# Performance work log

Measured on AMD Instinct MI355X. Metric: run time of the kernel, lower is better.

Reference implementation:

```python
import jax, jax.numpy as jnp
import numpy as np

M = 2          # n_mix
D_K = 128      # feature dim
TEMP = float(np.sqrt(D_K))  # temperature = d_k ** 0.5


def setup_inputs() -> dict:
    key = jax.random.key(0)
    k1, k2, k3, k4 = jax.random.split(key, 4)
    BS, N, N2 = 8, 2048, 2048
    qt = jax.random.normal(k1, (BS, N, D_K), jnp.float32)
    kt = jax.random.normal(k2, (BS, N2, D_K), jnp.float32)
    vt = jax.random.normal(k3, (BS, N2, D_K), jnp.float32)
    std = M ** -0.5
    kernel = jax.random.uniform(k4, (M, D_K), jnp.float32, -std, std)
    return {"qt": qt, "kt": kt, "vt": vt, "kernel": kernel}


def reference(qt, kt, vt, kernel):
    # channels_last path of MixtureOfSoftMaxACF.call, training=False (dropout = identity)
    BS, N, dk = qt.shape
    N2 = kt.shape[1]
    d = dk // M
    # mixture prior: softmax(kernel @ mean_q^T) over axis=1 (faithful to Softmax(axis=1))
    bar_qt = jnp.mean(qt, axis=1)                       # (BS, dk)
    prior_mix = jax.nn.softmax(kernel @ bar_qt.T, axis=1)  # (m, BS)
    prior_mix = prior_mix.reshape(BS * M, 1, 1)            # row-major reshape, as in TF
    # split features into mixtures via row-major reshape (as tf.reshape does)
    q = qt.reshape(BS * M, N, d)
    k = kt.reshape(BS * M, N2, d)
    att = jnp.einsum('bnd,bmd->bnm', q, k) / TEMP        # (BS*m, N, N2)
    att = jax.nn.softmax(att, axis=2)
    att = (att * prior_mix).reshape(BS, M, N, N2).sum(axis=1)  # (BS, N, N2)
    return att @ vt                                      # (BS, N, d_v)
```

## Files before the change

kernel.cpp:

```cpp
#include <hip/hip_runtime.h>
#include <hip/hip_fp16.h>

typedef float    f32x4 __attribute__((ext_vector_type(4)));
typedef _Float16 f16x2 __attribute__((ext_vector_type(2)));
typedef _Float16 f16x4 __attribute__((ext_vector_type(4)));
typedef _Float16 f16x8 __attribute__((ext_vector_type(8)));

#define BS 8
#define NN 2048
#define DK 128
#define DM 64
#define MIXOFF (1024 * DK)
#define QSCALE 0.12751744116926208f

#define MFMA32(a, b, c) __builtin_amdgcn_mfma_f32_16x16x32_f16((a), (b), (c), 0, 0, 0)
#define EXP2(x) __builtin_amdgcn_exp2f(x)

__device__ __forceinline__ f16x2 pkrtz(float x, float y) {
  return __builtin_bit_cast(f16x2, __builtin_amdgcn_cvt_pkrtz(x, y));
}

__device__ __forceinline__ void load_lds16(const _Float16* g, _Float16* l) {
  __builtin_amdgcn_global_load_lds(
      (const __attribute__((address_space(1))) void*)(uintptr_t)g,
      (__attribute__((address_space(3))) void*)(uint32_t)(uintptr_t)l, 16, 0, 0);
}

__global__ void prep_k(const float* __restrict__ kt, _Float16* __restrict__ kh,
                       const float* __restrict__ vt, _Float16* __restrict__ vT,
                       const float* __restrict__ qt, float* __restrict__ qpart) {
  __shared__ float tile[64][65];
  __shared__ float red[256];
  int blk = blockIdx.x;
  int t = threadIdx.x;
  if (blk < 512) {
    size_t base = (size_t)blk * 4096;
#pragma unroll
    for (int j = 0; j < 4; ++j) {
      size_t i = base + j * 1024 + t * 4;
      f32x4 v = *(const f32x4*)(kt + i);
      f16x4 h;
      h[0] = (_Float16)v[0]; h[1] = (_Float16)v[1];
      h[2] = (_Float16)v[2]; h[3] = (_Float16)v[3];
      *(f16x4*)(kh + i) = h;
    }
  } else if (blk < 1024) {
    int i2 = blk - 512;
    int b = i2 >> 6;
    int rem = i2 & 63;
    int j0 = (rem & 31) * 64;
    int c0 = (rem >> 5) * 64;
    int tx = t & 63, ty = t >> 6;
    const float* src = vt + ((size_t)b * NN + j0) * DK + c0;
#pragma unroll
    for (int rr = 0; rr < 16; ++rr) {
      int row = ty * 16 + rr;
      tile[row][tx] = src[(size_t)row * DK + tx];
    }
    __syncthreads();
    _Float16* dst = vT + ((size_t)b * DK + c0) * NN + j0;
    int chl = t >> 4;
    int k4 = (t & 15) * 4;
#pragma unroll
    for (int r2 = 0; r2 < 4; ++r2) {
      int ch = r2 * 16 + chl;
      f16x4 h;
      h[0] = (_Float16)tile[k4 + 0][ch]; h[1] = (_Float16)tile[k4 + 1][ch];
      h[2] = (_Float16)tile[k4 + 2][ch]; h[3] = (_Float16)tile[k4 + 3][ch];
      *(f16x4*)(dst + (size_t)ch * NN + k4) = h;
    }
  } else {
    int i = blk - 1024;
    int b = i >> 3, seg = i & 7;
    int c = t & 127, h = t >> 7;
    const float* p = qt + ((size_t)b * NN + seg * 256 + h * 128) * DK + c;
    float s = 0.f;
#pragma unroll 8
    for (int n = 0; n < 128; ++n) s += p[(size_t)n * DK];
    red[t] = s;
    __syncthreads();
    if (t < 128) qpart[(size_t)i * 128 + t] = red[t] + red[t + 128];
  }
}

#define STAGE(BUF, S) do {                                                 \
    _Float16* db_ = stg + (BUF) * 32768;                                   \
    load_lds16(khg + gKst + (S) * 2048,          db_ + t * 8);             \
    load_lds16(khg + gKst + 32768 + (S) * 2048,  db_ + 4096 + t * 8);      \
    load_lds16(khg + gKst + 65536 + (S) * 2048,  db_ + 8192 + t * 8);      \
    load_lds16(khg + gKst + 98304 + (S) * 2048,  db_ + 12288 + t * 8);     \
    load_lds16(vTg + gVst + (S) * 32,            db_ + 16384 + t * 8);     \
    load_lds16(vTg + gVst + 512 + (S) * 32,      db_ + 20480 + t * 8);     \
    load_lds16(vTg + gVst + 1024 + (S) * 32,     db_ + 24576 + t * 8);     \
    load_lds16(vTg + gVst + 1536 + (S) * 32,     db_ + 28672 + t * 8);     \
  } while (0)

__global__ __launch_bounds__(512, 2) void attn_k(const float* __restrict__ qt,
                                                 const _Float16* __restrict__ khg,
                                                 const _Float16* __restrict__ vTg,
                                                 const float* __restrict__ kern,
                                                 const float* __restrict__ qpart,
                                                 float* __restrict__ out) {
  __shared__ __align__(16) char smem[131072];
  _Float16* stg = (_Float16*)smem;
  const int b = blockIdx.x & 7;
  const int qb = blockIdx.x >> 3;
  const int t = threadIdx.x;
  const int wv = t >> 6;
  const int m = wv >> 2;
  const int kq = wv & 3;
  const int lane = t & 63;
  const int quad = lane >> 4, l16 = lane & 15;
  const int perm = ((l16 >> 2) << 3) | (l16 & 3);
  const int bq = b * (NN * DK);
  const int bV = b * (DK * NN);

  f16x8 qf[4][2];
#pragma unroll
  for (int su = 0; su < 4; ++su)
#pragma unroll
    for (int c = 0; c < 2; ++c) {
      const float* qp_ = qt + bq + m * MIXOFF +
                         (qb * 64 + su * 16 + l16) * DM + quad * 8 + c * 32;
      f32x4 v0 = *(const f32x4*)qp_;
      f32x4 v1 = *(const f32x4*)(qp_ + 4);
      union { f16x8 v; f16x2 h[4]; } w;
      w.h[0] = pkrtz(v0[0] * QSCALE, v0[1] * QSCALE);
      w.h[1] = pkrtz(v0[2] * QSCALE, v0[3] * QSCALE);
      w.h[2] = pkrtz(v1[0] * QSCALE, v1[1] * QSCALE);
      w.h[3] = pkrtz(v1[2] * QSCALE, v1[3] * QSCALE);
      qf[su][c] = w.v;
    }

  const int mixu = t >> 8;
  const int qq8 = t & 255;
  const int rK = qq8 >> 3;
  const int uuK = (qq8 & 7) ^ ((rK & 3) ^ (((rK >> 3) & 1) << 2));
  const int chV = t >> 2;
  const int uuV = (t & 3) ^ ((chV + (chV >> 2)) & 3);
  const int gKst = bq + mixu * MIXOFF + rK * 64 + uuK * 8;
  const int gVst = bV + chV * NN + uuV * 8;

  const int gK = (l16 & 3) ^ (((l16 >> 2) & 1) << 2);
  const int hV = (l16 + (l16 >> 2)) & 3;
  const int kA = (quad ^ gK) * 8;
  const int kB = ((quad + 4) ^ gK) * 8;
  const int kbase = kq * 4096 + m * 2048 + perm * 64;
  const int vbase = 16384 + kq * 4096 + l16 * 32 + (quad ^ hV) * 8;

  const f32x4 z = {0.f, 0.f, 0.f, 0.f};
  f32x4 acc[4][8];
  float lsum[4] = {0.f, 0.f, 0.f, 0.f};
#pragma unroll
  for (int su = 0; su < 4; ++su)
#pragma unroll
    for (int cc = 0; cc < 8; ++cc) acc[su][cc] = z;

  STAGE(0, 0);
  int buf = 0;
  for (int s = 0; s < 16; ++s) {
    __syncthreads();
    if (s + 1 < 16) STAGE(buf ^ 1, s + 1);
    const _Float16* sb_ = stg + buf * 32768;
    const _Float16* kb_ = sb_ + kbase;
    f16x8 kf0 = *(const f16x8*)(kb_ + kA);
    f16x8 kf1 = *(const f16x8*)(kb_ + kB);
    f16x8 kf2 = *(const f16x8*)(kb_ + 256 + kA);
    f16x8 kf3 = *(const f16x8*)(kb_ + 256 + kB);
    f16x8 pw[4];
#pragma unroll
    for (int su = 0; su < 4; ++su) {
      f32x4 s0 = MFMA32(kf1, qf[su][1], MFMA32(kf0, qf[su][0], z));
      f32x4 s1 = MFMA32(kf3, qf[su][1], MFMA32(kf2, qf[su][0], z));
      float e0 = EXP2(s0[0]), e1 = EXP2(s0[1]), e2 = EXP2(s0[2]), e3 = EXP2(s0[3]);
      float e4 = EXP2(s1[0]), e5 = EXP2(s1[1]), e6 = EXP2(s1[2]), e7 = EXP2(s1[3]);
      lsum[su] += ((e0 + e1) + (e2 + e3)) + ((e4 + e5) + (e6 + e7));
      union { f16x8 v; f16x2 h[4]; } w;
      w.h[0] = pkrtz(e0, e1); w.h[1] = pkrtz(e2, e3);
      w.h[2] = pkrtz(e4, e5); w.h[3] = pkrtz(e6, e7);
      pw[su] = w.v;
    }
    const _Float16* vb_ = sb_ + vbase;
#pragma unroll
    for (int cc = 0; cc < 8; ++cc) {
      f16x8 vf = *(const f16x8*)(vb_ + cc * 512);
#pragma unroll
      for (int su = 0; su < 4; ++su) acc[su][cc] = MFMA32(vf, pw[su], acc[su][cc]);
    }
    buf ^= 1;
  }
  __syncthreads();

  float* obuf0 = (float*)smem;
  float* obuf1 = (float*)(smem + 33792);
  float* barL = (float*)(smem + 67584);
  float* lgp = (float*)(smem + 71680);
  float* exq = (float*)(smem + 71744);
  float* prp = (float*)(smem + 71808);
  float* lbuf = (float*)(smem + 71936);

#pragma unroll
  for (int su = 0; su < 4; ++su) {
    lsum[su] += __shfl_xor(lsum[su], 16);
    lsum[su] += __shfl_xor(lsum[su], 32);
  }
  for (int e = t; e < 1024; e += 512) {
    int bb = e >> 7, c = e & 127;
    float ss = 0.f;
#pragma unroll
    for (int seg = 0; seg < 8; ++seg) ss += qpart[(size_t)(bb * 8 + seg) * 128 + c];
    barL[e] = ss * (1.0f / 2048.0f);
  }
  if (quad == 0)
#pragma unroll
    for (int su = 0; su < 4; ++su) lbuf[wv * 64 + su * 16 + l16] = lsum[su];
  __syncthreads();
  if (t < 16) {
    int mm = t >> 3, bb = t & 7;
    float ss = 0.f;
    for (int c = 0; c < DK; ++c) ss += kern[mm * DK + c] * barL[bb * 128 + c];
    lgp[t] = ss;
  }
  __syncthreads();
  if (t < 16) {
    int mm = t >> 3;
    float mx = lgp[mm * 8];
    for (int i = 1; i < 8; ++i) mx = fmaxf(mx, lgp[mm * 8 + i]);
    exq[t] = __expf(lgp[t] - mx);
  }
  __syncthreads();
  if (t < 16) {
    int mm = t >> 3;
    float sm = 0.f;
    for (int i = 0; i < 8; ++i) sm += exq[mm * 8 + i];
    prp[t] = exq[t] / sm;
  }
  __syncthreads();

  const float wm = prp[b * 2 + m];
  float rr[4];
#pragma unroll
  for (int su = 0; su < 4; ++su) {
    int q = su * 16 + l16;
    rr[su] = wm / (((lbuf[(m * 4 + 0) * 64 + q] + lbuf[(m * 4 + 1) * 64 + q]) +
                    (lbuf[(m * 4 + 2) * 64 + q] + lbuf[(m * 4 + 3) * 64 + q])));
  }

  float* ob = (m == 0) ? obuf0 : obuf1;
  if (kq == 0) {
#pragma unroll
    for (int su = 0; su < 4; ++su) {
      int r_ = (su * 16 + l16) * 132 + quad * 4;
#pragma unroll
      for (int cc = 0; cc < 8; ++cc) {
        f32x4 o;
#pragma unroll
        for (int e = 0; e < 4; ++e) o[e] = acc[su][cc][e] * rr[su];
        *(f32x4*)&ob[r_ + cc * 16] = o;
      }
    }
  }
  __syncthreads();
  for (int ph = 1; ph < 4; ++ph) {
    if (kq == ph) {
#pragma unroll
      for (int su = 0; su < 4; ++su) {
        int r_ = (su * 16 + l16) * 132 + quad * 4;
#pragma unroll
        for (int cc = 0; cc < 8; ++cc) {
          f32x4 o = *(const f32x4*)&ob[r_ + cc * 16];
#pragma unroll
          for (int e = 0; e < 4; ++e) o[e] += acc[su][cc][e] * rr[su];
          *(f32x4*)&ob[r_ + cc * 16] = o;
        }
      }
    }
    __syncthreads();
  }

  const int row = t >> 3;
  const int cb = (t & 7) * 16;
  float* op = out + ((size_t)b * NN + qb * 64 + row) * DK + cb;
#pragma unroll
  for (int g = 0; g < 4; ++g) {
    f32x4 a = *(const f32x4*)&obuf0[row * 132 + cb + g * 4];
    f32x4 c = *(const f32x4*)&obuf1[row * 132 + cb + g * 4];
#pragma unroll
    for (int e = 0; e < 4; ++e) a[e] += c[e];
    *(f32x4*)(op + g * 4) = a;
  }
}

extern "C" void kernel_launch(void* const* d_in, const int* in_sizes, int n_in,
                              void* d_out, int out_size, void* d_ws, size_t ws_size,
                              hipStream_t stream) {
  const float* qt = (const float*)d_in[0];
  const float* kt = (const float*)d_in[1];
  const float* vt = (const float*)d_in[2];
  const float* kern = (const float*)d_in[3];
  float* out = (float*)d_out;

  char* ws = (char*)d_ws;
  float* qpart = (float*)(ws + 4096);
  _Float16* khp = (_Float16*)(ws + 65536);
  _Float16* vTp = khp + (size_t)BS * NN * DK;

  prep_k<<<dim3(1088), dim3(256), 0, stream>>>(kt, khp, vt, vTp, qt, qpart);
  attn_k<<<dim3(256), dim3(512), 0, stream>>>(qt, khp, vTp, kern, qpart, out);
}
```

Before: 119.2 us.

## Double attention block to 1024 threads, splitting query rows across wave pairs

The attention kernel now runs 16 waves per block instead of 8. Each wave pair splits the 64 query rows of a block, so each wave holds 2 row subtiles of accumulators instead of 4, and the K and V staging loads are divided between the two thread halves. The aim is lower register pressure per wave and more waves in flight to hide MFMA, exp and LDS latency. In exchange, K fragments are read from LDS twice as often per block, the output tile is rewritten per thread, and launch bounds drop to one block per CU, since the 128 KB of shared memory already limited residency.

```diff
diff --git a/kernel.cpp b/kernel.cpp
--- a/kernel.cpp
+++ b/kernel.cpp
@@ -84,44 +84,48 @@
 }
 
 #define STAGE(BUF, S) do {                                                 \
-    _Float16* db_ = stg + (BUF) * 32768;                                   \
-    load_lds16(khg + gKst + (S) * 2048,          db_ + t * 8);             \
-    load_lds16(khg + gKst + 32768 + (S) * 2048,  db_ + 4096 + t * 8);      \
-    load_lds16(khg + gKst + 65536 + (S) * 2048,  db_ + 8192 + t * 8);      \
-    load_lds16(khg + gKst + 98304 + (S) * 2048,  db_ + 12288 + t * 8);     \
-    load_lds16(vTg + gVst + (S) * 32,            db_ + 16384 + t * 8);     \
-    load_lds16(vTg + gVst + 512 + (S) * 32,      db_ + 20480 + t * 8);     \
-    load_lds16(vTg + gVst + 1024 + (S) * 32,     db_ + 24576 + t * 8);     \
-    load_lds16(vTg + gVst + 1536 + (S) * 32,     db_ + 28672 + t * 8);     \
+    _Float16* db_ = stg + (BUF) * 32768 + i * 8;                           \
+    if (!isV) {                                                            \
+      load_lds16(khg + gKst + (S) * 2048,          db_);                   \
+      load_lds16(khg + gKst + 32768 + (S) * 2048,  db_ + 4096);            \
+      load_lds16(khg + gKst + 65536 + (S) * 2048,  db_ + 8192);            \
+      load_lds16(khg + gKst + 98304 + (S) * 2048,  db_ + 12288);           \
+    } else {                                                               \
+      load_lds16(vTg + gVst + (S) * 32,            db_ + 16384);           \
+      load_lds16(vTg + gVst + 512 + (S) * 32,      db_ + 20480);           \
+      load_lds16(vTg + gVst + 1024 + (S) * 32,     db_ + 24576);           \
+      load_lds16(vTg + gVst + 1536 + (S) * 32,     db_ + 28672);           \
+    }                                                                      \
   } while (0)
 
-__global__ __launch_bounds__(512, 2) void attn_k(const float* __restrict__ qt,
-                                                 const _Float16* __restrict__ khg,
-                                                 const _Float16* __restrict__ vTg,
-                                                 const float* __restrict__ kern,
-                                                 const float* __restrict__ qpart,
-                                                 float* __restrict__ out) {
+__global__ __launch_bounds__(1024, 1) void attn_k(const float* __restrict__ qt,
+                                                  const _Float16* __restrict__ khg,
+                                                  const _Float16* __restrict__ vTg,
+                                                  const float* __restrict__ kern,
+                                                  const float* __restrict__ qpart,
+                                                  float* __restrict__ out) {
   __shared__ __align__(16) char smem[131072];
   _Float16* stg = (_Float16*)smem;
   const int b = blockIdx.x & 7;
   const int qb = blockIdx.x >> 3;
   const int t = threadIdx.x;
   const int wv = t >> 6;
-  const int m = wv >> 2;
-  const int kq = wv & 3;
+  const int m = wv >> 3;
+  const int kq = (wv >> 1) & 3;
+  const int u = wv & 1;
   const int lane = t & 63;
   const int quad = lane >> 4, l16 = lane & 15;
   const int perm = ((l16 >> 2) << 3) | (l16 & 3);
   const int bq = b * (NN * DK);
   const int bV = b * (DK * NN);
 
-  f16x8 qf[4][2];
-#pragma unroll
-  for (int su = 0; su < 4; ++su)
+  f16x8 qf[2][2];
+#pragma unroll
+  for (int su = 0; su < 2; ++su)
 #pragma unroll
     for (int c = 0; c < 2; ++c) {
       const float* qp_ = qt + bq + m * MIXOFF +
-                         (qb * 64 + su * 16 + l16) * DM + quad * 8 + c * 32;
+                         (qb * 64 + u * 32 + su * 16 + l16) * DM + quad * 8 + c * 32;
       f32x4 v0 = *(const f32x4*)qp_;
       f32x4 v1 = *(const f32x4*)(qp_ + 4);
       union { f16x8 v; f16x2 h[4]; } w;
@@ -132,12 +136,14 @@
       qf[su][c] = w.v;
     }
 
-  const int mixu = t >> 8;
-  const int qq8 = t & 255;
+  const int i = t & 511;
+  const int isV = t >> 9;
+  const int mixu = i >> 8;
+  const int qq8 = i & 255;
   const int rK = qq8 >> 3;
   const int uuK = (qq8 & 7) ^ ((rK & 3) ^ (((rK >> 3) & 1) << 2));
-  const int chV = t >> 2;
-  const int uuV = (t & 3) ^ ((chV + (chV >> 2)) & 3);
+  const int chV = i >> 2;
+  const int uuV = (i & 3) ^ ((chV + (chV >> 2)) & 3);
   const int gKst = bq + mixu * MIXOFF + rK * 64 + uuK * 8;
   const int gVst = bV + chV * NN + uuV * 8;
 
@@ -149,10 +155,10 @@
   const int vbase = 16384 + kq * 4096 + l16 * 32 + (quad ^ hV) * 8;
 
   const f32x4 z = {0.f, 0.f, 0.f, 0.f};
-  f32x4 acc[4][8];
-  float lsum[4] = {0.f, 0.f, 0.f, 0.f};
-#pragma unroll
-  for (int su = 0; su < 4; ++su)
+  f32x4 acc[2][8];
+  float lsum[2] = {0.f, 0.f};
+#pragma unroll
+  for (int su = 0; su < 2; ++su)
 #pragma unroll
     for (int cc = 0; cc < 8; ++cc) acc[su][cc] = z;
 
@@ -167,9 +173,9 @@
     f16x8 kf1 = *(const f16x8*)(kb_ + kB);
     f16x8 kf2 = *(const f16x8*)(kb_ + 256 + kA);
     f16x8 kf3 = *(const f16x8*)(kb_ + 256 + kB);
-    f16x8 pw[4];
-#pragma unroll
-    for (int su = 0; su < 4; ++su) {
+    f16x8 pw[2];
+#pragma unroll
+    for (int su = 0; su < 2; ++su) {
       f32x4 s0 = MFMA32(kf1, qf[su][1], MFMA32(kf0, qf[su][0], z));
       f32x4 s1 = MFMA32(kf3, qf[su][1], MFMA32(kf2, qf[su][0], z));
       float e0 = EXP2(s0[0]), e1 = EXP2(s0[1]), e2 = EXP2(s0[2]), e3 = EXP2(s0[3]);
@@ -185,7 +191,7 @@
     for (int cc = 0; cc < 8; ++cc) {
       f16x8 vf = *(const f16x8*)(vb_ + cc * 512);
 #pragma unroll
-      for (int su = 0; su < 4; ++su) acc[su][cc] = MFMA32(vf, pw[su], acc[su][cc]);
+      for (int su = 0; su < 2; ++su) acc[su][cc] = MFMA32(vf, pw[su], acc[su][cc]);
     }
     buf ^= 1;
   }
@@ -200,20 +206,21 @@
   float* lbuf = (float*)(smem + 71936);
 
 #pragma unroll
-  for (int su = 0; su < 4; ++su) {
+  for (int su = 0; su < 2; ++su) {
     lsum[su] += __shfl_xor(lsum[su], 16);
     lsum[su] += __shfl_xor(lsum[su], 32);
   }
-  for (int e = t; e < 1024; e += 512) {
-    int bb = e >> 7, c = e & 127;
+  {
+    int bb = t >> 7, c = t & 127;
     float ss = 0.f;
 #pragma unroll
     for (int seg = 0; seg < 8; ++seg) ss += qpart[(size_t)(bb * 8 + seg) * 128 + c];
-    barL[e] = ss * (1.0f / 2048.0f);
+    barL[t] = ss * (1.0f / 2048.0f);
   }
   if (quad == 0)
 #pragma unroll
-    for (int su = 0; su < 4; ++su) lbuf[wv * 64 + su * 16 + l16] = lsum[su];
+    for (int su = 0; su < 2; ++su)
+      lbuf[(m * 4 + kq) * 64 + u * 32 + su * 16 + l16] = lsum[su];
   __syncthreads();
   if (t < 16) {
     int mm = t >> 3, bb = t & 7;
@@ -225,23 +232,23 @@
   if (t < 16) {
     int mm = t >> 3;
     float mx = lgp[mm * 8];
-    for (int i = 1; i < 8; ++i) mx = fmaxf(mx, lgp[mm * 8 + i]);
+    for (int i2 = 1; i2 < 8; ++i2) mx = fmaxf(mx, lgp[mm * 8 + i2]);
     exq[t] = __expf(lgp[t] - mx);
   }
   __syncthreads();
   if (t < 16) {
     int mm = t >> 3;
     float sm = 0.f;
-    for (int i = 0; i < 8; ++i) sm += exq[mm * 8 + i];
+    for (int i2 = 0; i2 < 8; ++i2) sm += exq[mm * 8 + i2];
     prp[t] = exq[t] / sm;
   }
   __syncthreads();
 
   const float wm = prp[b * 2 + m];
-  float rr[4];
-#pragma unroll
-  for (int su = 0; su < 4; ++su) {
-    int q = su * 16 + l16;
+  float rr[2];
+#pragma unroll
+  for (int su = 0; su < 2; ++su) {
+    int q = u * 32 + su * 16 + l16;
     rr[su] = wm / (((lbuf[(m * 4 + 0) * 64 + q] + lbuf[(m * 4 + 1) * 64 + q]) +
                     (lbuf[(m * 4 + 2) * 64 + q] + lbuf[(m * 4 + 3) * 64 + q])));
   }
@@ -249,8 +256,8 @@
   float* ob = (m == 0) ? obuf0 : obuf1;
   if (kq == 0) {
 #pragma unroll
-    for (int su = 0; su < 4; ++su) {
-      int r_ = (su * 16 + l16) * 132 + quad * 4;
+    for (int su = 0; su < 2; ++su) {
+      int r_ = (u * 32 + su * 16 + l16) * 132 + quad * 4;
 #pragma unroll
       for (int cc = 0; cc < 8; ++cc) {
         f32x4 o;
@@ -264,8 +271,8 @@
   for (int ph = 1; ph < 4; ++ph) {
     if (kq == ph) {
 #pragma unroll
-      for (int su = 0; su < 4; ++su) {
-        int r_ = (su * 16 + l16) * 132 + quad * 4;
+      for (int su = 0; su < 2; ++su) {
+        int r_ = (u * 32 + su * 16 + l16) * 132 + quad * 4;
 #pragma unroll
         for (int cc = 0; cc < 8; ++cc) {
           f32x4 o = *(const f32x4*)&ob[r_ + cc * 16];
@@ -278,11 +285,11 @@
     __syncthreads();
   }
 
-  const int row = t >> 3;
-  const int cb = (t & 7) * 16;
+  const int row = t >> 4;
+  const int cb = (t & 15) * 8;
   float* op = out + ((size_t)b * NN + qb * 64 + row) * DK + cb;
 #pragma unroll
-  for (int g = 0; g < 4; ++g) {
+  for (int g = 0; g < 2; ++g) {
     f32x4 a = *(const f32x4*)&obuf0[row * 132 + cb + g * 4];
     f32x4 c = *(const f32x4*)&obuf1[row * 132 + cb + g * 4];
 #pragma unroll
@@ -306,5 +313,5 @@
   _Float16* vTp = khp + (size_t)BS * NN * DK;
 
   prep_k<<<dim3(1088), dim3(256), 0, stream>>>(kt, khp, vt, vTp, qt, qpart);
-  attn_k<<<dim3(256), dim3(512), 0, stream>>>(qt, khp, vTp, kern, qpart, out);
-}
+  attn_k<<<dim3(256), dim3(1024), 0, stream>>>(qt, khp, vTp, kern, qpart, out);
+}
```

Result: slower. 123.4 us (+3.5%).

## Halve query tile per block and read V directly from global memory

Applied to the files above, without the earlier changes.

Each block now handles 32 query rows instead of 64 and launches twice as many blocks. Only K is staged in LDS (8 KB per buffer), while V fragments are loaded straight from global/L2 into registers, which cuts LDS to 40 KB and raises occupancy to 4 blocks per CU. The key dimension is split across 2 waves instead of 4, over 32 stages. This trades reuse for parallelism: each V fragment now feeds one MFMA instead of four, so global/L2 traffic for V rises and there is less MFMA work per load.

```diff
diff --git a/kernel.cpp b/kernel.cpp
--- a/kernel.cpp
+++ b/kernel.cpp
@@ -84,126 +84,104 @@
 }
 
 #define STAGE(BUF, S) do {                                                 \
-    _Float16* db_ = stg + (BUF) * 32768;                                   \
+    _Float16* db_ = stg + (BUF) * 8192;                                    \
     load_lds16(khg + gKst + (S) * 2048,          db_ + t * 8);             \
-    load_lds16(khg + gKst + 32768 + (S) * 2048,  db_ + 4096 + t * 8);      \
-    load_lds16(khg + gKst + 65536 + (S) * 2048,  db_ + 8192 + t * 8);      \
-    load_lds16(khg + gKst + 98304 + (S) * 2048,  db_ + 12288 + t * 8);     \
-    load_lds16(vTg + gVst + (S) * 32,            db_ + 16384 + t * 8);     \
-    load_lds16(vTg + gVst + 512 + (S) * 32,      db_ + 20480 + t * 8);     \
-    load_lds16(vTg + gVst + 1024 + (S) * 32,     db_ + 24576 + t * 8);     \
-    load_lds16(vTg + gVst + 1536 + (S) * 32,     db_ + 28672 + t * 8);     \
+    load_lds16(khg + gKst + 65536 + (S) * 2048,  db_ + 4096 + t * 8);      \
   } while (0)
 
-__global__ __launch_bounds__(512, 2) void attn_k(const float* __restrict__ qt,
+__global__ __launch_bounds__(512, 4) void attn_k(const float* __restrict__ qt,
                                                  const _Float16* __restrict__ khg,
                                                  const _Float16* __restrict__ vTg,
                                                  const float* __restrict__ kern,
                                                  const float* __restrict__ qpart,
                                                  float* __restrict__ out) {
-  __shared__ __align__(16) char smem[131072];
+  __shared__ __align__(16) char smem[40960];
   _Float16* stg = (_Float16*)smem;
   const int b = blockIdx.x & 7;
   const int qb = blockIdx.x >> 3;
   const int t = threadIdx.x;
   const int wv = t >> 6;
   const int m = wv >> 2;
-  const int kq = wv & 3;
+  const int kh = (wv >> 1) & 1;
+  const int u = wv & 1;
   const int lane = t & 63;
   const int quad = lane >> 4, l16 = lane & 15;
   const int perm = ((l16 >> 2) << 3) | (l16 & 3);
   const int bq = b * (NN * DK);
   const int bV = b * (DK * NN);
 
-  f16x8 qf[4][2];
-#pragma unroll
-  for (int su = 0; su < 4; ++su)
-#pragma unroll
-    for (int c = 0; c < 2; ++c) {
-      const float* qp_ = qt + bq + m * MIXOFF +
-                         (qb * 64 + su * 16 + l16) * DM + quad * 8 + c * 32;
-      f32x4 v0 = *(const f32x4*)qp_;
-      f32x4 v1 = *(const f32x4*)(qp_ + 4);
-      union { f16x8 v; f16x2 h[4]; } w;
-      w.h[0] = pkrtz(v0[0] * QSCALE, v0[1] * QSCALE);
-      w.h[1] = pkrtz(v0[2] * QSCALE, v0[3] * QSCALE);
-      w.h[2] = pkrtz(v1[0] * QSCALE, v1[1] * QSCALE);
-      w.h[3] = pkrtz(v1[2] * QSCALE, v1[3] * QSCALE);
-      qf[su][c] = w.v;
-    }
+  f16x8 qf[2];
+#pragma unroll
+  for (int c = 0; c < 2; ++c) {
+    const float* qp_ = qt + bq + m * MIXOFF +
+                       (qb * 32 + u * 16 + l16) * DM + quad * 8 + c * 32;
+    f32x4 v0 = *(const f32x4*)qp_;
+    f32x4 v1 = *(const f32x4*)(qp_ + 4);
+    union { f16x8 v; f16x2 h[4]; } w;
+    w.h[0] = pkrtz(v0[0] * QSCALE, v0[1] * QSCALE);
+    w.h[1] = pkrtz(v0[2] * QSCALE, v0[3] * QSCALE);
+    w.h[2] = pkrtz(v1[0] * QSCALE, v1[1] * QSCALE);
+    w.h[3] = pkrtz(v1[2] * QSCALE, v1[3] * QSCALE);
+    qf[c] = w.v;
+  }
 
   const int mixu = t >> 8;
   const int qq8 = t & 255;
   const int rK = qq8 >> 3;
   const int uuK = (qq8 & 7) ^ ((rK & 3) ^ (((rK >> 3) & 1) << 2));
-  const int chV = t >> 2;
-  const int uuV = (t & 3) ^ ((chV + (chV >> 2)) & 3);
   const int gKst = bq + mixu * MIXOFF + rK * 64 + uuK * 8;
-  const int gVst = bV + chV * NN + uuV * 8;
 
   const int gK = (l16 & 3) ^ (((l16 >> 2) & 1) << 2);
-  const int hV = (l16 + (l16 >> 2)) & 3;
   const int kA = (quad ^ gK) * 8;
   const int kB = ((quad + 4) ^ gK) * 8;
-  const int kbase = kq * 4096 + m * 2048 + perm * 64;
-  const int vbase = 16384 + kq * 4096 + l16 * 32 + (quad ^ hV) * 8;
+  const int kbase = kh * 4096 + m * 2048 + perm * 64;
+
+  const _Float16* vpb = vTg + (size_t)bV + (size_t)l16 * NN + kh * 1024 + quad * 8;
 
   const f32x4 z = {0.f, 0.f, 0.f, 0.f};
-  f32x4 acc[4][8];
-  float lsum[4] = {0.f, 0.f, 0.f, 0.f};
-#pragma unroll
-  for (int su = 0; su < 4; ++su)
-#pragma unroll
-    for (int cc = 0; cc < 8; ++cc) acc[su][cc] = z;
+  f32x4 acc[8];
+  float lsum = 0.f;
+#pragma unroll
+  for (int cc = 0; cc < 8; ++cc) acc[cc] = z;
 
   STAGE(0, 0);
   int buf = 0;
-  for (int s = 0; s < 16; ++s) {
+  for (int s = 0; s < 32; ++s) {
     __syncthreads();
-    if (s + 1 < 16) STAGE(buf ^ 1, s + 1);
-    const _Float16* sb_ = stg + buf * 32768;
-    const _Float16* kb_ = sb_ + kbase;
+    if (s + 1 < 32) STAGE(buf ^ 1, s + 1);
+    f16x8 vf[8];
+#pragma unroll
+    for (int cc = 0; cc < 8; ++cc)
+      vf[cc] = *(const f16x8*)(vpb + (size_t)cc * 16 * NN + s * 32);
+    const _Float16* kb_ = stg + buf * 8192 + kbase;
     f16x8 kf0 = *(const f16x8*)(kb_ + kA);
     f16x8 kf1 = *(const f16x8*)(kb_ + kB);
     f16x8 kf2 = *(const f16x8*)(kb_ + 256 + kA);
     f16x8 kf3 = *(const f16x8*)(kb_ + 256 + kB);
-    f16x8 pw[4];
-#pragma unroll
-    for (int su = 0; su < 4; ++su) {
-      f32x4 s0 = MFMA32(kf1, qf[su][1], MFMA32(kf0, qf[su][0], z));
-      f32x4 s1 = MFMA32(kf3, qf[su][1], MFMA32(kf2, qf[su][0], z));
-      float e0 = EXP2(s0[0]), e1 = EXP2(s0[1]), e2 = EXP2(s0[2]), e3 = EXP2(s0[3]);
-      float e4 = EXP2(s1[0]), e5 = EXP2(s1[1]), e6 = EXP2(s1[2]), e7 = EXP2(s1[3]);
-      lsum[su] += ((e0 + e1) + (e2 + e3)) + ((e4 + e5) + (e6 + e7));
-      union { f16x8 v; f16x2 h[4]; } w;
-      w.h[0] = pkrtz(e0, e1); w.h[1] = pkrtz(e2, e3);
-      w.h[2] = pkrtz(e4, e5); w.h[3] = pkrtz(e6, e7);
-      pw[su] = w.v;
-    }
-    const _Float16* vb_ = sb_ + vbase;
-#pragma unroll
-    for (int cc = 0; cc < 8; ++cc) {
-      f16x8 vf = *(const f16x8*)(vb_ + cc * 512);
-#pragma unroll
-      for (int su = 0; su < 4; ++su) acc[su][cc] = MFMA32(vf, pw[su], acc[su][cc]);
-    }
+    f32x4 s0 = MFMA32(kf1, qf[1], MFMA32(kf0, qf[0], z));
+    f32x4 s1 = MFMA32(kf3, qf[1], MFMA32(kf2, qf[0], z));
+    float e0 = EXP2(s0[0]), e1 = EXP2(s0[1]), e2 = EXP2(s0[2]), e3 = EXP2(s0[3]);
+    float e4 = EXP2(s1[0]), e5 = EXP2(s1[1]), e6 = EXP2(s1[2]), e7 = EXP2(s1[3]);
+    lsum += ((e0 + e1) + (e2 + e3)) + ((e4 + e5) + (e6 + e7));
+    union { f16x8 v; f16x2 h[4]; } w;
+    w.h[0] = pkrtz(e0, e1); w.h[1] = pkrtz(e2, e3);
+    w.h[2] = pkrtz(e4, e5); w.h[3] = pkrtz(e6, e7);
+#pragma unroll
+    for (int cc = 0; cc < 8; ++cc) acc[cc] = MFMA32(vf[cc], w.v, acc[cc]);
     buf ^= 1;
   }
   __syncthreads();
 
   float* obuf0 = (float*)smem;
-  float* obuf1 = (float*)(smem + 33792);
-  float* barL = (float*)(smem + 67584);
-  float* lgp = (float*)(smem + 71680);
-  float* exq = (float*)(smem + 71744);
-  float* prp = (float*)(smem + 71808);
-  float* lbuf = (float*)(smem + 71936);
-
-#pragma unroll
-  for (int su = 0; su < 4; ++su) {
-    lsum[su] += __shfl_xor(lsum[su], 16);
-    lsum[su] += __shfl_xor(lsum[su], 32);
-  }
+  float* obuf1 = (float*)(smem + 16896);
+  float* barL = (float*)(smem + 33792);
+  float* lgp = (float*)(smem + 37888);
+  float* exq = (float*)(smem + 37952);
+  float* prp = (float*)(smem + 38016);
+  float* lbuf = (float*)(smem + 38080);
+
+  lsum += __shfl_xor(lsum, 16);
+  lsum += __shfl_xor(lsum, 32);
   for (int e = t; e < 1024; e += 512) {
     int bb = e >> 7, c = e & 127;
     float ss = 0.f;
@@ -211,9 +189,7 @@
     for (int seg = 0; seg < 8; ++seg) ss += qpart[(size_t)(bb * 8 + seg) * 128 + c];
     barL[e] = ss * (1.0f / 2048.0f);
   }
-  if (quad == 0)
-#pragma unroll
-    for (int su = 0; su < 4; ++su) lbuf[wv * 64 + su * 16 + l16] = lsum[su];
+  if (quad == 0) lbuf[(m * 2 + kh) * 32 + u * 16 + l16] = lsum;
   __syncthreads();
   if (t < 16) {
     int mm = t >> 3, bb = t & 7;
@@ -225,64 +201,51 @@
   if (t < 16) {
     int mm = t >> 3;
     float mx = lgp[mm * 8];
-    for (int i = 1; i < 8; ++i) mx = fmaxf(mx, lgp[mm * 8 + i]);
+    for (int i2 = 1; i2 < 8; ++i2) mx = fmaxf(mx, lgp[mm * 8 + i2]);
     exq[t] = __expf(lgp[t] - mx);
   }
   __syncthreads();
   if (t < 16) {
     int mm = t >> 3;
     float sm = 0.f;
-    for (int i = 0; i < 8; ++i) sm += exq[mm * 8 + i];
+    for (int i2 = 0; i2 < 8; ++i2) sm += exq[mm * 8 + i2];
     prp[t] = exq[t] / sm;
   }
   __syncthreads();
 
   const float wm = prp[b * 2 + m];
-  float rr[4];
-#pragma unroll
-  for (int su = 0; su < 4; ++su) {
-    int q = su * 16 + l16;
-    rr[su] = wm / (((lbuf[(m * 4 + 0) * 64 + q] + lbuf[(m * 4 + 1) * 64 + q]) +
-                    (lbuf[(m * 4 + 2) * 64 + q] + lbuf[(m * 4 + 3) * 64 + q])));
-  }
+  const int q = u * 16 + l16;
+  const float rr = wm / (lbuf[(m * 2 + 0) * 32 + q] + lbuf[(m * 2 + 1) * 32 + q]);
 
   float* ob = (m == 0) ? obuf0 : obuf1;
-  if (kq == 0) {
-#pragma unroll
-    for (int su = 0; su < 4; ++su) {
-      int r_ = (su * 16 + l16) * 132 + quad * 4;
-#pragma unroll
-      for (int cc = 0; cc < 8; ++cc) {
-        f32x4 o;
-#pragma unroll
-        for (int e = 0; e < 4; ++e) o[e] = acc[su][cc][e] * rr[su];
-        *(f32x4*)&ob[r_ + cc * 16] = o;
-      }
-    }
-  }
-  __syncthreads();
-  for (int ph = 1; ph < 4; ++ph) {
-    if (kq == ph) {
-#pragma unroll
-      for (int su = 0; su < 4; ++su) {
-        int r_ = (su * 16 + l16) * 132 + quad * 4;
-#pragma unroll
-        for (int cc = 0; cc < 8; ++cc) {
-          f32x4 o = *(const f32x4*)&ob[r_ + cc * 16];
-#pragma unroll
-          for (int e = 0; e < 4; ++e) o[e] += acc[su][cc][e] * rr[su];
-          *(f32x4*)&ob[r_ + cc * 16] = o;
-        }
-      }
-    }
-    __syncthreads();
-  }
-
-  const int row = t >> 3;
-  const int cb = (t & 7) * 16;
-  float* op = out + ((size_t)b * NN + qb * 64 + row) * DK + cb;
-#pragma unroll
-  for (int g = 0; g < 4; ++g) {
+  if (kh == 0) {
+    int r_ = q * 132 + quad * 4;
+#pragma unroll
+    for (int cc = 0; cc < 8; ++cc) {
+      f32x4 o;
+#pragma unroll
+      for (int e = 0; e < 4; ++e) o[e] = acc[cc][e] * rr;
+      *(f32x4*)&ob[r_ + cc * 16] = o;
+    }
+  }
+  __syncthreads();
+  if (kh == 1) {
+    int r_ = q * 132 + quad * 4;
+#pragma unroll
+    for (int cc = 0; cc < 8; ++cc) {
+      f32x4 o = *(const f32x4*)&ob[r_ + cc * 16];
+#pragma unroll
+      for (int e = 0; e < 4; ++e) o[e] += acc[cc][e] * rr;
+      *(f32x4*)&ob[r_ + cc * 16] = o;
+    }
+  }
+  __syncthreads();
+
+  const int row = t >> 4;
+  const int cb = (t & 15) * 8;
+  float* op = out + ((size_t)b * NN + qb * 32 + row) * DK + cb;
+#pragma unroll
+  for (int g = 0; g < 2; ++g) {
     f32x4 a = *(const f32x4*)&obuf0[row * 132 + cb + g * 4];
     f32x4 c = *(const f32x4*)&obuf1[row * 132 + cb + g * 4];
 #pragma unroll
@@ -306,5 +269,5 @@
   _Float16* vTp = khp + (size_t)BS * NN * DK;
 
   prep_k<<<dim3(1088), dim3(256), 0, stream>>>(kt, khp, vt, vTp, qt, qpart);
-  attn_k<<<dim3(256), dim3(512), 0, stream>>>(qt, khp, vTp, kern, qpart, out);
-}
+  attn_k<<<dim3(512), dim3(512), 0, stream>>>(qt, khp, vTp, kern, qpart, out);
+}
```

Result: slower. 207.9 us (+74.4%).
